# Kernel tuning notes

Measured on AMD Instinct MI355X. Metric: run time of the kernel, lower is better.

## Reference

```python
import jax, jax.numpy as jnp
import numpy as np


def setup_inputs() -> dict:
    key = jax.random.key(0)
    k1, k2, k3, k4 = jax.random.split(key, 4)
    B, C, L = 16, 512, 4096
    x = jax.random.normal(k1, (B, C, L), dtype=jnp.float32)
    # conv1d kernel_size=1, bias=False -> weight [3C, C]
    w_qkv = jax.random.normal(k2, (3 * C, C), dtype=jnp.float32) * (1.0 / np.sqrt(C))
    w_out = jax.random.normal(k3, (C, C), dtype=jnp.float32) * (1.0 / np.sqrt(C))
    b_out = jax.random.normal(k4, (C,), dtype=jnp.float32) * 0.01
    return {"x": x, "w_qkv": w_qkv, "w_out": w_out, "b_out": b_out}


def reference(x, w_qkv, w_out, b_out):
    # x: [b, c, l]; 1x1 conv == channel-wise matmul
    qkv = jnp.einsum('bcl,oc->bol', x, w_qkv)          # [b, 3c, l]
    q, k, v = jnp.split(qkv, 3, axis=1)                 # each [b, c, l] (heads=1)
    k = jax.nn.softmax(k, axis=-1)                      # softmax over sequence dim l
    context = jnp.einsum('bdn,ben->bde', k, v)          # [b, c, c]
    out = jnp.einsum('bde,bdn->ben', context, q)        # [b, c, l]
    return jnp.einsum('bcl,oc->bol', out, w_out) + b_out[None, :, None]
```

## Files before the change

### kernel.cpp

```cpp
#include <hip/hip_runtime.h>
#include <hip/hip_bf16.h>
#include <type_traits>

#define DEVINL __device__ __forceinline__

typedef float f32x4 __attribute__((ext_vector_type(4)));
typedef __bf16 bf16x8 __attribute__((ext_vector_type(8)));

DEVINL float bf2f(short s) {
  unsigned u = ((unsigned)(unsigned short)s) << 16;
  float f; __builtin_memcpy(&f, &u, 4); return f;
}
DEVINL short f2bf(float f) {
  unsigned u; __builtin_memcpy(&u, &f, 4);
  u += 0x7fff + ((u >> 16) & 1);
  return (short)(u >> 16);
}

DEVINL void gl_lds16(const void* g, void* l) {
  __builtin_amdgcn_global_load_lds(
      (const __attribute__((address_space(1))) void*)g,
      (__attribute__((address_space(3))) void*)l, 16, 0, 0);
}

DEVINL void swz_blk(int& bx, int& by, int& bz) {
  const int gx = gridDim.x, gy = gridDim.y;
  const int tpz = gx * gy;
  const int nwg = tpz * gridDim.z;
  int fid = bx + gx * (by + gy * bz);
  fid = (fid & 7) * (nwg >> 3) + (fid >> 3);
  bz = fid / tpz;
  const int r = fid - bz * tpz;
  by = r % gy;
  bx = r / gy;
}

template <typename OutT, bool BIAS, bool EXP>
DEVINL void epilogue_store(f32x4 (&acc)[4][4], char* smem,
                           OutT* __restrict__ C, int ldc, int m0, int n0,
                           const float* __restrict__ bias,
                           float* __restrict__ rowsum, int t) {
  const int wave = t >> 6, lane = t & 63;
  const int quad = lane >> 4, l16 = lane & 15;
  const int arow = (wave >> 1) * 64, brow = (wave & 1) * 64;
  if constexpr (std::is_same<OutT, float>::value) {
    float* tile = (float*)smem;
#pragma unroll
    for (int rnd = 0; rnd < 2; ++rnd) {
      if ((arow >> 6) == rnd) {
#pragma unroll
        for (int mi = 0; mi < 4; ++mi)
#pragma unroll
          for (int ni = 0; ni < 4; ++ni) {
            const int col = brow + ni * 16 + l16;
#pragma unroll
            for (int r = 0; r < 4; ++r) {
              const int row = mi * 16 + quad * 4 + r;
              float v = acc[mi][ni][r];
              if (BIAS) v += bias[m0 + rnd * 64 + row];
              tile[row * 128 + col] = v;
            }
          }
      }
      __syncthreads();
#pragma unroll
      for (int i = 0; i < 8; ++i) {
        const int row = wave * 16 + i * 2 + (lane >> 5);
        const int cf  = (lane & 31) * 4;
        f32x4 v = *(f32x4*)&tile[row * 128 + cf];
        *(f32x4*)&C[(long)(m0 + rnd * 64 + row) * ldc + n0 + cf] = v;
      }
      __syncthreads();
    }
  } else {
    short* tile = (short*)smem;
#pragma unroll
    for (int mi = 0; mi < 4; ++mi)
#pragma unroll
      for (int r = 0; r < 4; ++r) {
        const int row = arow + mi * 16 + quad * 4 + r;
        float rs = 0.f;
#pragma unroll
        for (int ni = 0; ni < 4; ++ni) {
          const int col = brow + ni * 16 + l16;
          float v = acc[mi][ni][r];
          if (BIAS) v += bias[m0 + row];
          if (EXP) { v = __expf(v); rs += v; }
          tile[row * 128 + col] = f2bf(v);
        }
        if (EXP) {
          rs += __shfl_xor(rs, 1); rs += __shfl_xor(rs, 2);
          rs += __shfl_xor(rs, 4); rs += __shfl_xor(rs, 8);
          if (l16 == 0) atomicAdd(&rowsum[m0 + row], rs);
        }
      }
    __syncthreads();
#pragma unroll
    for (int i = 0; i < 8; ++i) {
      const int row = wave * 32 + i * 4 + (lane >> 4);
      const int cs  = l16 * 8;
      int4 v = *(int4*)&tile[row * 128 + cs];
      *(int4*)&C[(long)(m0 + row) * ldc + n0 + cs] = v;
    }
  }
}

#define GEMM_K_LOOP(A_, lda_, B_, ldb_, kbeg_, kend_)                        \
  {                                                                          \
    const int lrow = t >> 2;                                                 \
    const int lk8  = (t & 3) * 8;                                            \
    auto stage = [&](int buf, int k0) {                                      \
      _Pragma("unroll")                                                      \
      for (int s = 0; s < 2; ++s) {                                          \
        gl_lds16(A_ + (long)(m0 + s * 64 + lrow) * lda_ + k0 + lk8,          \
                 smem + buf * 16384 + s * 4096 + wave * 1024);               \
        gl_lds16(B_ + (long)(n0 + s * 64 + lrow) * ldb_ + k0 + lk8,          \
                 smem + buf * 16384 + 8192 + s * 4096 + wave * 1024);        \
      }                                                                      \
    };                                                                       \
    stage(0, kbeg_);                                                         \
    __syncthreads();                        \
    int cur = 0;                                                             \
    for (int k0 = kbeg_; k0 < kend_; k0 += 32) {                             \
      if (k0 + 32 < kend_) stage(cur ^ 1, k0 + 32);        \
      const short* As = (const short*)(smem + cur * 16384);                  \
      const short* Bs = (const short*)(smem + cur * 16384 + 8192);           \
      bf16x8 af[4], bfr[4];                                                  \
      _Pragma("unroll")                                                      \
      for (int i = 0; i < 4; ++i)                                            \
        af[i] = *(const bf16x8*)&As[(arow + i * 16 + l16) * 32 + quad * 8];  \
      _Pragma("unroll")                                                      \
      for (int i = 0; i < 4; ++i)                                            \
        bfr[i] = *(const bf16x8*)&Bs[(brow + i * 16 + l16) * 32 + quad * 8]; \
      _Pragma("unroll")                                                      \
      for (int mi = 0; mi < 4; ++mi)                                         \
        _Pragma("unroll")                                                    \
        for (int ni = 0; ni < 4; ++ni)                                       \
          acc[mi][ni] = __builtin_amdgcn_mfma_f32_16x16x32_bf16(             \
              af[mi], bfr[ni], acc[mi][ni], 0, 0, 0);                        \
      __syncthreads();                    \
      cur ^= 1;                                                              \
    }                                                                        \
  }

template <typename OutT, bool BIAS, bool EXP>
__global__ __launch_bounds__(256, 4)
void gemm_nt(const short* __restrict__ A, long sA, int lda,
             const short* __restrict__ B, long sB, int ldb,
             OutT* __restrict__ C, long sC, int ldc,
             const float* __restrict__ bias, float* __restrict__ rowsum, int K)
{
  int bx = blockIdx.x, by = blockIdx.y, bz = blockIdx.z;
  swz_blk(bx, by, bz);

  A += (long)bz * sA;
  B += (long)bz * sB;
  C += (long)bz * sC;
  if (EXP) rowsum += (long)bz * 512;

  __shared__ char smem[32768];

  const int t    = threadIdx.x;
  const int wave = t >> 6, lane = t & 63;
  const int quad = lane >> 4, l16 = lane & 15;
  const int m0 = by * 128, n0 = bx * 128;
  const int arow = (wave >> 1) * 64, brow = (wave & 1) * 64;

  f32x4 acc[4][4];
#pragma unroll
  for (int i = 0; i < 4; ++i)
#pragma unroll
    for (int j = 0; j < 4; ++j) acc[i][j] = (f32x4){0.f, 0.f, 0.f, 0.f};

  GEMM_K_LOOP(A, lda, B, ldb, 0, K)

  epilogue_store<OutT, BIAS, EXP>(acc, smem, C, ldc, m0, n0, bias, rowsum, t);
}

__global__ __launch_bounds__(256, 4)
void gemm_sk(const short* __restrict__ Ab, const short* __restrict__ Bb,
             float* __restrict__ Cp)
{
  int bx = blockIdx.x, by = blockIdx.y, bz = blockIdx.z;
  swz_blk(bx, by, bz);

  const int b = bz >> 2, s = bz & 3;
  const short* A = Ab + (long)b * 2097152;
  const short* B = Bb + (long)b * 2097152;
  float* C = Cp + (long)(s * 16 + b) * 262144;

  __shared__ char smem[32768];

  const int t    = threadIdx.x;
  const int wave = t >> 6, lane = t & 63;
  const int quad = lane >> 4, l16 = lane & 15;
  const int m0 = by * 128, n0 = bx * 128;
  const int arow = (wave >> 1) * 64, brow = (wave & 1) * 64;
  const int kbeg = s * 1024, kend = kbeg + 1024;

  f32x4 acc[4][4];
#pragma unroll
  for (int i = 0; i < 4; ++i)
#pragma unroll
    for (int j = 0; j < 4; ++j) acc[i][j] = (f32x4){0.f, 0.f, 0.f, 0.f};

  GEMM_K_LOOP(A, 4096, B, 4096, kbeg, kend)

  epilogue_store<float, false, false>(acc, smem, C, 512, m0, n0, nullptr,
                                      nullptr, t);
}

__global__ void reduce_sk(const float* __restrict__ p, short* __restrict__ o,
                          const float* __restrict__ s) {
  const long i = ((long)blockIdx.x * 256 + threadIdx.x) * 4;
  const float inv = 1.f / s[i >> 9];
  f32x4 a = *(const f32x4*)&p[i];
  f32x4 b = *(const f32x4*)&p[i + 4194304];
  f32x4 c = *(const f32x4*)&p[i + 2 * 4194304];
  f32x4 d = *(const f32x4*)&p[i + 3 * 4194304];
  short r[4];
#pragma unroll
  for (int j = 0; j < 4; ++j) r[j] = f2bf((a[j] + b[j] + c[j] + d[j]) * inv);
  *(long*)&o[i] = *(long*)r;
}

__global__ void transpose_cast(const float* __restrict__ x,
                               short* __restrict__ xT, short* __restrict__ xb)
{
  __shared__ short tile[64][73];
  x  += (long)blockIdx.z * 2097152;
  xT += (long)blockIdx.z * 2097152;
  xb += (long)blockIdx.z * 2097152;
  const int l0 = blockIdx.x * 64, c0 = blockIdx.y * 64;
  const int t  = threadIdx.x;
  const int rr = t >> 4;
  const int q4 = (t & 15) * 4;
#pragma unroll
  for (int i = 0; i < 4; ++i) {
    const int r = rr + i * 16;
    f32x4 v = *(const f32x4*)&x[(long)(c0 + r) * 4096 + l0 + q4];
    short s4[4];
#pragma unroll
    for (int j = 0; j < 4; ++j) s4[j] = f2bf(v[j]);
    *(long*)&xb[(long)(c0 + r) * 4096 + l0 + q4] = *(long*)s4;
#pragma unroll
    for (int j = 0; j < 4; ++j) tile[r][q4 + j] = s4[j];
  }
  __syncthreads();
#pragma unroll
  for (int i = 0; i < 4; ++i) {
    const int l = rr + i * 16;
    short o4[4];
#pragma unroll
    for (int j = 0; j < 4; ++j) o4[j] = tile[q4 + j][l];
    *(long*)&xT[(long)(l0 + l) * 512 + c0 + q4] = *(long*)o4;
  }
}

DEVINL float to_f(float v) { return v; }
DEVINL float to_f(short v) { return bf2f(v); }

template <typename InT, typename OutT>
__global__ void transpose_k(const InT* __restrict__ src, OutT* __restrict__ dst,
                            int R, int Cc, long ss, long ds)
{
  __shared__ float tile[32][33];
  src += (long)blockIdx.z * ss;
  dst += (long)blockIdx.z * ds;
  const int c0 = blockIdx.x * 32, r0 = blockIdx.y * 32;
  const int tx = threadIdx.x, ty = threadIdx.y;
#pragma unroll
  for (int i = 0; i < 4; ++i)
    tile[ty + i * 8][tx] = to_f(src[(long)(r0 + ty + i * 8) * Cc + c0 + tx]);
  __syncthreads();
#pragma unroll
  for (int i = 0; i < 4; ++i) {
    float v = tile[tx][ty + i * 8];
    if constexpr (std::is_same<OutT, float>::value)
      dst[(long)(c0 + ty + i * 8) * R + r0 + tx] = v;
    else
      dst[(long)(c0 + ty + i * 8) * R + r0 + tx] = f2bf(v);
  }
}

__global__ void cast_weights(const float* __restrict__ wq, short* __restrict__ wqb,
                             const float* __restrict__ wo, short* __restrict__ wob,
                             float* __restrict__ ssum) {
  const int i = blockIdx.x * 256 + threadIdx.x;
  if (blockIdx.x < 32) ssum[i] = 0.f;
  if (i < 786432) wqb[i] = f2bf(wq[i]);
  else            wob[i - 786432] = f2bf(wo[i - 786432]);
}

extern "C" void kernel_launch(void* const* d_in, const int* in_sizes, int n_in,
                              void* d_out, int out_size, void* d_ws, size_t ws_size,
                              hipStream_t stream) {
  const float* x     = (const float*)d_in[0];
  const float* w_qkv = (const float*)d_in[1];
  const float* w_out = (const float*)d_in[2];
  const float* b_out = (const float*)d_in[3];
  float* out = (float*)d_out;

  const long CL = (long)512 * 4096;
  const long CC = (long)512 * 512;

  char* ws = (char*)d_ws;
  short* xT  = (short*)(ws);
  short* xb  = (short*)(ws + 67108864);
  short* kbf = (short*)(ws + 134217728);
  float* Pp  = (float*)(ws + 201326592);
  short* P   = (short*)(ws + 268435456);
  short* ctx = (short*)(ws + 276824064);
  short* M2  = (short*)(ws + 285212672);
  short* M3  = (short*)(ws + 293601280);
  short* wqb = (short*)(ws + 301989888);
  short* wob = (short*)(ws + 303562752);
  short* wqT = (short*)(ws + 304087040);
  float* ssum = (float*)(ws + 293601280);

  cast_weights<<<4096, 256, 0, stream>>>(w_qkv, wqb, w_out, wob, ssum);

  transpose_k<float, short><<<dim3(16, 16, 1), dim3(32, 8), 0, stream>>>(
      w_qkv, wqT, 512, 512, 0, 0);

  transpose_cast<<<dim3(64, 8, 16), 256, 0, stream>>>(x, xT, xb);

  gemm_nt<short, false, true><<<dim3(32, 4, 16), 256, 0, stream>>>(
      wqb + 512 * 512, 0, 512, xT, CL, 512, kbf, CL, 4096, nullptr, ssum, 512);

  gemm_sk<<<dim3(4, 4, 64), 256, 0, stream>>>(kbf, xb, Pp);
  reduce_sk<<<4096, 256, 0, stream>>>(Pp, P, ssum);

  gemm_nt<short, false, false><<<dim3(4, 4, 16), 256, 0, stream>>>(
      P, CC, 512, wqb + 2 * 512 * 512, 0, 512, ctx, CC, 512, nullptr, nullptr, 512);

  gemm_nt<short, false, false><<<dim3(4, 4, 16), 256, 0, stream>>>(
      wob, 0, 512, ctx, CC, 512, M2, CC, 512, nullptr, nullptr, 512);

  gemm_nt<short, false, false><<<dim3(4, 4, 16), 256, 0, stream>>>(
      M2, CC, 512, wqT, 0, 512, M3, CC, 512, nullptr, nullptr, 512);

  gemm_nt<float, true, false><<<dim3(32, 4, 16), 256, 0, stream>>>(
      M3, CC, 512, xT, CL, 512, out, CL, 4096, b_out, nullptr, 512);
}
```

Before: 493.8 us.

## Widen big GEMM tiles to 128x256 and fold value weights into output weight

Adds a 512-thread GEMM variant with 128x256 output tiles (8 waves), used for the key projection, the split-K context GEMM and the final output GEMM. It is meant to cut redundant A-tile loads and improve operand reuse. It also precomputes U = W_out·W_v^T once, which removes one batched 512x512 GEMM per batch from the chain. The cost is more shared memory per block, a different rounding order for the folded product, and larger blocks that may lower occupancy.

```diff
diff --git a/kernel.cpp b/kernel.cpp
--- a/kernel.cpp
+++ b/kernel.cpp
@@ -34,6 +34,7 @@
   by = r % gy;
   bx = r / gy;
 }
+
 
 template <typename OutT, bool BIAS, bool EXP>
 DEVINL void epilogue_store(f32x4 (&acc)[4][4], char* smem,
@@ -119,10 +120,10 @@
       }                                                                      \
     };                                                                       \
     stage(0, kbeg_);                                                         \
-    __syncthreads();                        \
+    __syncthreads();                                                         \
     int cur = 0;                                                             \
     for (int k0 = kbeg_; k0 < kend_; k0 += 32) {                             \
-      if (k0 + 32 < kend_) stage(cur ^ 1, k0 + 32);        \
+      if (k0 + 32 < kend_) stage(cur ^ 1, k0 + 32);                          \
       const short* As = (const short*)(smem + cur * 16384);                  \
       const short* Bs = (const short*)(smem + cur * 16384 + 8192);           \
       bf16x8 af[4], bfr[4];                                                  \
@@ -138,7 +139,7 @@
         for (int ni = 0; ni < 4; ++ni)                                       \
           acc[mi][ni] = __builtin_amdgcn_mfma_f32_16x16x32_bf16(             \
               af[mi], bfr[ni], acc[mi][ni], 0, 0, 0);                        \
-      __syncthreads();                    \
+      __syncthreads();                                                       \
       cur ^= 1;                                                              \
     }                                                                        \
   }
@@ -177,9 +178,170 @@
   epilogue_store<OutT, BIAS, EXP>(acc, smem, C, ldc, m0, n0, bias, rowsum, t);
 }
 
-__global__ __launch_bounds__(256, 4)
-void gemm_sk(const short* __restrict__ Ab, const short* __restrict__ Bb,
-             float* __restrict__ Cp)
+
+template <typename OutT, bool BIAS, bool EXP>
+DEVINL void epilogue_store_wide(f32x4 (&acc)[4][4], char* smem,
+                                OutT* __restrict__ C, int ldc, int m0, int n0,
+                                const float* __restrict__ bias,
+                                float* __restrict__ rowsum, int t) {
+  const int wave = t >> 6, lane = t & 63;
+  const int quad = lane >> 4, l16 = lane & 15;
+  const int arow = (wave >> 2) * 64, brow = (wave & 3) * 64;
+  const int rn_w = brow >> 7;
+  const int colb = brow & 64;
+  if constexpr (std::is_same<OutT, float>::value) {
+    float* tile = (float*)smem;
+    const int rm_w = arow >> 6;
+#pragma unroll
+    for (int rm = 0; rm < 2; ++rm)
+#pragma unroll
+      for (int rn = 0; rn < 2; ++rn) {
+        if (rm_w == rm && rn_w == rn) {
+#pragma unroll
+          for (int mi = 0; mi < 4; ++mi)
+#pragma unroll
+            for (int ni = 0; ni < 4; ++ni)
+#pragma unroll
+              for (int r = 0; r < 4; ++r) {
+                const int row = mi * 16 + quad * 4 + r;
+                float v = acc[mi][ni][r];
+                if (BIAS) v += bias[m0 + rm * 64 + row];
+                tile[row * 128 + colb + ni * 16 + l16] = v;
+              }
+        }
+        __syncthreads();
+#pragma unroll
+        for (int i = 0; i < 4; ++i) {
+          const int row = wave * 8 + i * 2 + (lane >> 5);
+          const int cf  = (lane & 31) * 4;
+          *(f32x4*)&C[(long)(m0 + rm * 64 + row) * ldc + n0 + rn * 128 + cf] =
+              *(f32x4*)&tile[row * 128 + cf];
+        }
+        __syncthreads();
+      }
+  } else {
+    if (EXP) {
+#pragma unroll
+      for (int mi = 0; mi < 4; ++mi)
+#pragma unroll
+        for (int r = 0; r < 4; ++r) {
+          const int row = arow + mi * 16 + quad * 4 + r;
+          float rs = 0.f;
+#pragma unroll
+          for (int ni = 0; ni < 4; ++ni) {
+            float v = __expf(acc[mi][ni][r]);
+            acc[mi][ni][r] = v; rs += v;
+          }
+          rs += __shfl_xor(rs, 1); rs += __shfl_xor(rs, 2);
+          rs += __shfl_xor(rs, 4); rs += __shfl_xor(rs, 8);
+          if (l16 == 0) atomicAdd(&rowsum[m0 + row], rs);
+        }
+    }
+    short* tile = (short*)smem;
+#pragma unroll
+    for (int rn = 0; rn < 2; ++rn) {
+      if (rn_w == rn) {
+#pragma unroll
+        for (int mi = 0; mi < 4; ++mi)
+#pragma unroll
+          for (int ni = 0; ni < 4; ++ni)
+#pragma unroll
+            for (int r = 0; r < 4; ++r) {
+              const int row = arow + mi * 16 + quad * 4 + r;
+              float v = acc[mi][ni][r];
+              if (BIAS) v += bias[m0 + row];
+              tile[row * 128 + colb + ni * 16 + l16] = f2bf(v);
+            }
+      }
+      __syncthreads();
+#pragma unroll
+      for (int i = 0; i < 4; ++i) {
+        const int row = wave * 16 + i * 4 + (lane >> 4);
+        const int cs  = l16 * 8;
+        *(int4*)&C[(long)(m0 + row) * ldc + n0 + rn * 128 + cs] =
+            *(int4*)&tile[row * 128 + cs];
+      }
+      __syncthreads();
+    }
+  }
+}
+
+#define WIDE_K_LOOP(A_, lda_, B_, ldb_, kbeg_, kend_)                        \
+  {                                                                          \
+    const int lrow = t >> 2;                                     \
+    const int lk8  = (t & 3) * 8;                                            \
+    auto stage = [&](int buf, int k0) {                                      \
+      gl_lds16(A_ + (long)(m0 + lrow) * lda_ + k0 + lk8,                     \
+               smem + buf * 24576 + wave * 1024);                            \
+      _Pragma("unroll")                                                      \
+      for (int s = 0; s < 2; ++s)                                            \
+        gl_lds16(B_ + (long)(n0 + s * 128 + lrow) * ldb_ + k0 + lk8,         \
+                 smem + buf * 24576 + 8192 + s * 8192 + wave * 1024);        \
+    };                                                                       \
+    stage(0, kbeg_);                                                         \
+    __syncthreads();                                                         \
+    int cur = 0;                                                             \
+    for (int k0 = kbeg_; k0 < kend_; k0 += 32) {                             \
+      if (k0 + 32 < kend_) stage(cur ^ 1, k0 + 32);                          \
+      const short* As = (const short*)(smem + cur * 24576);                  \
+      const short* Bs = (const short*)(smem + cur * 24576 + 8192);           \
+      bf16x8 af[4], bfr[4];                                                  \
+      _Pragma("unroll")                                                      \
+      for (int i = 0; i < 4; ++i)                                            \
+        af[i] = *(const bf16x8*)&As[(arow + i * 16 + l16) * 32 + quad * 8];  \
+      _Pragma("unroll")                                                      \
+      for (int i = 0; i < 4; ++i)                                            \
+        bfr[i] = *(const bf16x8*)&Bs[(brow + i * 16 + l16) * 32 + quad * 8]; \
+      _Pragma("unroll")                                                      \
+      for (int mi = 0; mi < 4; ++mi)                                         \
+        _Pragma("unroll")                                                    \
+        for (int ni = 0; ni < 4; ++ni)                                       \
+          acc[mi][ni] = __builtin_amdgcn_mfma_f32_16x16x32_bf16(             \
+              af[mi], bfr[ni], acc[mi][ni], 0, 0, 0);                        \
+      __syncthreads();                                                       \
+      cur ^= 1;                                                              \
+    }                                                                        \
+  }
+
+template <typename OutT, bool BIAS, bool EXP>
+__global__ __launch_bounds__(512, 4)
+void gemm_nt_wide(const short* __restrict__ A, long sA, int lda,
+                  const short* __restrict__ B, long sB, int ldb,
+                  OutT* __restrict__ C, long sC, int ldc,
+                  const float* __restrict__ bias, float* __restrict__ rowsum,
+                  int K)
+{
+  int bx = blockIdx.x, by = blockIdx.y, bz = blockIdx.z;
+  swz_blk(bx, by, bz);
+
+  A += (long)bz * sA;
+  B += (long)bz * sB;
+  C += (long)bz * sC;
+  if (EXP) rowsum += (long)bz * 512;
+
+  __shared__ char smem[49152];
+
+  const int t    = threadIdx.x;
+  const int wave = t >> 6, lane = t & 63;
+  const int quad = lane >> 4, l16 = lane & 15;
+  const int m0 = by * 128, n0 = bx * 256;
+  const int arow = (wave >> 2) * 64, brow = (wave & 3) * 64;
+
+  f32x4 acc[4][4];
+#pragma unroll
+  for (int i = 0; i < 4; ++i)
+#pragma unroll
+    for (int j = 0; j < 4; ++j) acc[i][j] = (f32x4){0.f, 0.f, 0.f, 0.f};
+
+  WIDE_K_LOOP(A, lda, B, ldb, 0, K)
+
+  epilogue_store_wide<OutT, BIAS, EXP>(acc, smem, C, ldc, m0, n0, bias,
+                                       rowsum, t);
+}
+
+__global__ __launch_bounds__(512, 4)
+void gemm_sk_wide(const short* __restrict__ Ab, const short* __restrict__ Bb,
+                  float* __restrict__ Cp)
 {
   int bx = blockIdx.x, by = blockIdx.y, bz = blockIdx.z;
   swz_blk(bx, by, bz);
@@ -189,13 +351,13 @@
   const short* B = Bb + (long)b * 2097152;
   float* C = Cp + (long)(s * 16 + b) * 262144;
 
-  __shared__ char smem[32768];
+  __shared__ char smem[49152];
 
   const int t    = threadIdx.x;
   const int wave = t >> 6, lane = t & 63;
   const int quad = lane >> 4, l16 = lane & 15;
-  const int m0 = by * 128, n0 = bx * 128;
-  const int arow = (wave >> 1) * 64, brow = (wave & 1) * 64;
+  const int m0 = by * 128, n0 = bx * 256;
+  const int arow = (wave >> 2) * 64, brow = (wave & 3) * 64;
   const int kbeg = s * 1024, kend = kbeg + 1024;
 
   f32x4 acc[4][4];
@@ -204,10 +366,10 @@
 #pragma unroll
     for (int j = 0; j < 4; ++j) acc[i][j] = (f32x4){0.f, 0.f, 0.f, 0.f};
 
-  GEMM_K_LOOP(A, 4096, B, 4096, kbeg, kend)
-
-  epilogue_store<float, false, false>(acc, smem, C, 512, m0, n0, nullptr,
-                                      nullptr, t);
+  WIDE_K_LOOP(A, 4096, B, 4096, kbeg, kend)
+
+  epilogue_store_wide<float, false, false>(acc, smem, C, 512, m0, n0, nullptr,
+                                           nullptr, t);
 }
 
 __global__ void reduce_sk(const float* __restrict__ p, short* __restrict__ o,
@@ -310,7 +472,8 @@
   short* kbf = (short*)(ws + 134217728);
   float* Pp  = (float*)(ws + 201326592);
   short* P   = (short*)(ws + 268435456);
-  short* ctx = (short*)(ws + 276824064);
+  short* U   = (short*)(ws + 276824064);
+  short* wvT = (short*)(ws + 277348352);
   short* M2  = (short*)(ws + 285212672);
   short* M3  = (short*)(ws + 293601280);
   short* wqb = (short*)(ws + 301989888);
@@ -322,24 +485,26 @@
 
   transpose_k<float, short><<<dim3(16, 16, 1), dim3(32, 8), 0, stream>>>(
       w_qkv, wqT, 512, 512, 0, 0);
+  transpose_k<short, short><<<dim3(16, 16, 1), dim3(32, 8), 0, stream>>>(
+      wqb + 2 * CC, wvT, 512, 512, 0, 0);
+
+  gemm_nt<short, false, false><<<dim3(4, 4, 1), 256, 0, stream>>>(
+      wob, 0, 512, wvT, 0, 512, U, 0, 512, nullptr, nullptr, 512);
 
   transpose_cast<<<dim3(64, 8, 16), 256, 0, stream>>>(x, xT, xb);
 
-  gemm_nt<short, false, true><<<dim3(32, 4, 16), 256, 0, stream>>>(
-      wqb + 512 * 512, 0, 512, xT, CL, 512, kbf, CL, 4096, nullptr, ssum, 512);
-
-  gemm_sk<<<dim3(4, 4, 64), 256, 0, stream>>>(kbf, xb, Pp);
+  gemm_nt_wide<short, false, true><<<dim3(16, 4, 16), 512, 0, stream>>>(
+      wqb + CC, 0, 512, xT, CL, 512, kbf, CL, 4096, nullptr, ssum, 512);
+
+  gemm_sk_wide<<<dim3(2, 4, 64), 512, 0, stream>>>(kbf, xb, Pp);
   reduce_sk<<<4096, 256, 0, stream>>>(Pp, P, ssum);
 
   gemm_nt<short, false, false><<<dim3(4, 4, 16), 256, 0, stream>>>(
-      P, CC, 512, wqb + 2 * 512 * 512, 0, 512, ctx, CC, 512, nullptr, nullptr, 512);
-
-  gemm_nt<short, false, false><<<dim3(4, 4, 16), 256, 0, stream>>>(
-      wob, 0, 512, ctx, CC, 512, M2, CC, 512, nullptr, nullptr, 512);
+      U, 0, 512, P, CC, 512, M2, CC, 512, nullptr, nullptr, 512);
 
   gemm_nt<short, false, false><<<dim3(4, 4, 16), 256, 0, stream>>>(
       M2, CC, 512, wqT, 0, 512, M3, CC, 512, nullptr, nullptr, 512);
 
-  gemm_nt<float, true, false><<<dim3(32, 4, 16), 256, 0, stream>>>(
+  gemm_nt_wide<float, true, false><<<dim3(16, 4, 16), 512, 0, stream>>>(
       M3, CC, 512, xT, CL, 512, out, CL, 4096, b_out, nullptr, 512);
 }
```

Result: no change. 487.9 us (-1.2%).
